# Kernel tuning notes

Measured on AMD Instinct MI355X. Metric: run time of the kernel, lower is better.

The kernel has to match this reference:

```python
import jax, jax.numpy as jnp
import numpy as np

ATT = 6  # att_size per axis
HEADS = 8

def leaky(x, s):
    return jnp.where(x >= 0, x, s * x)

def conv1x1(x, w, b):
    # x: [B,C,D,H,W], w: [O,C]
    return jnp.einsum('bcdhw,oc->bodhw', x, w) + b[None, :, None, None, None]

def conv3x3x3(x, w, b):
    y = jax.lax.conv_general_dilated(x, w, (1, 1, 1), [(1, 1)] * 3,
                                     dimension_numbers=('NCDHW', 'OIDHW', 'NCDHW'))
    return y + b[None, :, None, None, None]

def group_norm(x, g, b, groups=6, eps=1e-5):
    B, C = x.shape[:2]
    xr = x.reshape(B, groups, -1)
    m = xr.mean(-1, keepdims=True)
    v = xr.var(-1, keepdims=True)
    xr = (xr - m) * jax.lax.rsqrt(v + eps)
    return xr.reshape(x.shape) * g[None, :, None, None, None] + b[None, :, None, None, None]

def instance_norm(x, eps=1e-5):
    m = x.mean((2, 3, 4), keepdims=True)
    v = x.var((2, 3, 4), keepdims=True)
    return (x - m) * jax.lax.rsqrt(v + eps)

def pool_sum(x, out=ATT):
    # adaptive max + avg pool; spatial dims divisible by out -> exact block reduce
    B, C, D, H, W = x.shape
    f = D // out
    xr = x.reshape(B, C, out, f, out, f, out, f)
    return xr.max((3, 5, 7)) + xr.mean((3, 5, 7))

def interp_axis(x, axis, out_size):
    # 1D linear interp with align_corners=True
    in_size = x.shape[axis]
    pos = jnp.arange(out_size) * ((in_size - 1) / (out_size - 1))
    i0 = jnp.floor(pos).astype(jnp.int32)
    i1 = jnp.minimum(i0 + 1, in_size - 1)
    w = (pos - i0).astype(x.dtype)
    shp = [1] * x.ndim
    shp[axis] = out_size
    w = w.reshape(shp)
    return jnp.take(x, i0, axis=axis) * (1 - w) + jnp.take(x, i1, axis=axis) * w

def upsample_trilinear(x, size):
    for ax, s in zip((2, 3, 4), size):
        x = interp_axis(x, ax, s)
    return x

def lin_attn(q, k, v, wq, bq, wk, bk, wv, bv, wo, bo):
    # efficient (linear) cross-attention: softmax over feature dim for Q, token dim for K
    B, N, C = q.shape
    dh = C // HEADS
    qh = (jnp.einsum('bnc,oc->bno', q, wq) + bq).reshape(B, N, HEADS, dh)
    kh = (jnp.einsum('bnc,oc->bno', k, wk) + bk).reshape(B, N, HEADS, dh)
    vh = (jnp.einsum('bnc,oc->bno', v, wv) + bv).reshape(B, N, HEADS, dh)
    qs = jax.nn.softmax(qh, axis=-1)
    ks = jax.nn.softmax(kh, axis=1)
    ctx = jnp.einsum('bnhd,bnhe->bhde', ks, vh)      # [B,H,dh,dh]
    out = jnp.einsum('bnhd,bhde->bnhe', qs, ctx).reshape(B, N, C)
    out = jnp.einsum('bnc,oc->bno', out, wo) + bo
    return out.transpose(0, 2, 1)  # [B,C,N]

def deconv2(x, w, b):
    # ConvTranspose3d kernel=stride=2; w: [Cin,Cout,2,2,2]
    B, C, D, H, W = x.shape
    O = w.shape[1]
    y = jnp.einsum('bcdhw,coijk->bodihjwk', x, w).reshape(B, O, 2 * D, 2 * H, 2 * W)
    return y + b[None, :, None, None, None]

def setup_inputs():
    key = jax.random.key(0)
    ks = iter(jax.random.split(key, 48))
    nrm = lambda *s: jax.random.normal(next(ks), s, jnp.float32)
    w = lambda *s: nrm(*s) * 0.05
    d = {
        'x': nrm(4, 64, 24, 24, 24),
        'x_e': nrm(4, 32, 48, 48, 48),
        'up_w': w(64, 32, 2, 2, 2), 'up_b': w(32),
        'wf': w(48, 64), 'bf': w(48),
        'w1': w(48, 32), 'b1': w(48), 'w2': w(48, 32), 'b2': w(48),
        'w3': w(48, 48), 'b3': w(48), 'w4': w(48, 48), 'b4': w(48),
        'gn_g': jnp.ones(48, jnp.float32), 'gn_b': jnp.zeros(48, jnp.float32),
        'a1_wq': w(48, 48), 'a1_bq': w(48), 'a1_wk': w(48, 48), 'a1_bk': w(48),
        'a1_wv': w(48, 48), 'a1_bv': w(48), 'a1_wo': w(48, 48), 'a1_bo': w(48),
        'a2_wq': w(48, 48), 'a2_bq': w(48), 'a2_wk': w(48, 48), 'a2_bk': w(48),
        'a2_wv': w(48, 48), 'a2_bv': w(48), 'a2_wo': w(48, 48), 'a2_bo': w(48),
        'wfin': w(64, 96), 'bfin': w(64),
        'c0_w': w(32, 64, 3, 3, 3), 'c0_b': w(32),
        'c1_w': w(32, 32, 3, 3, 3), 'c1_b': w(32),
    }
    return d

def reference(x, x_e, up_w, up_b, wf, bf, w1, b1, w2, b2, w3, b3, w4, b4, gn_g, gn_b,
              a1_wq, a1_bq, a1_wk, a1_bk, a1_wv, a1_bv, a1_wo, a1_bo,
              a2_wq, a2_bq, a2_wk, a2_bk, a2_wv, a2_bv, a2_wo, a2_bo,
              wfin, bfin, c0_w, c0_b, c1_w, c1_b):
    x0 = deconv2(x, up_w, up_b)                                   # [B,32,48,48,48]
    fusion = conv1x1(jnp.concatenate([x_e, x0], 1), wf, bf)       # [B,48,...]
    B, C = fusion.shape[:2]
    i1 = leaky(group_norm(conv1x1(x0, w1, b1), gn_g, gn_b), 0.1)
    i1 = leaky(group_norm(conv1x1(i1, w3, b3), gn_g, gn_b), 0.1)
    i2 = leaky(group_norm(conv1x1(x_e, w2, b2), gn_g, gn_b), 0.1)
    i2 = leaky(group_norm(conv1x1(i2, w4, b4), gn_g, gn_b), 0.1)
    p1 = pool_sum(i1)
    p2 = pool_sum(i2)
    pkv = pool_sum(fusion)
    q1 = p1.reshape(B, C, -1).transpose(0, 2, 1)
    q2 = p2.reshape(B, C, -1).transpose(0, 2, 1)
    kv = pkv.reshape(B, C, -1).transpose(0, 2, 1)
    a1 = lin_attn(q1, kv, kv, a1_wq, a1_bq, a1_wk, a1_bk, a1_wv, a1_bv, a1_wo, a1_bo).reshape(B, C, ATT, ATT, ATT)
    a2 = lin_attn(q2, kv, kv, a2_wq, a2_bq, a2_wk, a2_bk, a2_wv, a2_bv, a2_wo, a2_bo).reshape(B, C, ATT, ATT, ATT)
    size = i1.shape[2:]
    o1 = jax.nn.sigmoid(upsample_trilinear(a1, size)) * i1
    o2 = jax.nn.sigmoid(upsample_trilinear(a2, size)) * i2
    out = conv1x1(jnp.concatenate([o1, o2], 1), wfin, bfin)       # [B,64,...]
    h = leaky(instance_norm(conv3x3x3(out, c0_w, c0_b)), 0.01)
    h = leaky(instance_norm(conv3x3x3(h, c1_w, c1_b)), 0.01)
    return h
```

## Files before the change

### kernel.cpp

```cpp
#include <hip/hip_runtime.h>
#include <hip/hip_bf16.h>

typedef __hip_bfloat16 bf16;
typedef __attribute__((ext_vector_type(8))) short short8x;
typedef __attribute__((ext_vector_type(4))) float f32x4;
typedef __attribute__((ext_vector_type(4))) unsigned int uint4x;

#define NV 110592
#define NVLL 110592ull
#define NSH 64
#define STSTRIDE 704

__device__ inline float ldmix(const void* p, size_t i, int f){
  return f ? ((const float*)p)[i] : __bfloat162float(((const bf16*)p)[i]);
}
__device__ inline float lo2f(unsigned int u){ union{unsigned int i; float f;} t; t.i = u<<16; return t.f; }
__device__ inline float hi2f(unsigned int u){ union{unsigned int i; float f;} t; t.i = u & 0xffff0000u; return t.f; }
__device__ inline unsigned short bfb(float f){ bf16 h=__float2bfloat16(f); unsigned short u; __builtin_memcpy(&u,&h,2); return u; }
__device__ inline unsigned int pk2(float a, float b){ return (unsigned int)bfb(a) | ((unsigned int)bfb(b)<<16); }

static const size_t BOFF_O1 = 2621440;
static const size_t BOFF_O2 = 45088768;
static const size_t BOFF_SP = 87556096;
static const size_t SLOT48  = 10616832;
#define SM_P1   0
#define SM_P2   41472
#define SM_PKV  82944
#define SM_A1   124416
#define SM_A2   165888
#define SM_ST   207360
#define SM_W    252416

#define W_UPW   0
#define W_UPB   16384
#define W_WF    16416
#define W_BF    19488
#define W_W1    19536
#define W_B1    21072
#define W_W2    21120
#define W_B2    22656
#define W_W3    22704
#define W_B3    25008
#define W_W4    25056
#define W_B4    27360
#define W_GNG   27408
#define W_GNB   27456
#define W_ATT   27504
#define W_WFIN  46320
#define W_BFIN  52464
#define W_C0W   52528
#define W_C0B   107824
#define W_C1W   107856
#define W_C1B   135504
#define W_TOTAL 135536
#define W_W1P   135536
#define W_B1F   160112
#define W_WFP   160160
#define W_BFF   184736
#define W_WP    184784
#define W_TB    267728
#define W_WB1   268592
#define W_WB2   310064
#define W_WB3   323888
#define W_WB4   324656
#define W_WB5   326192
#define W_WBI   327728
#define SM_FL   604720

__global__ __launch_bounds__(256) void k_detect(const void* xe, float* __restrict__ flag){
  const bf16* p = (const bf16*)xe;
  int tid = threadIdx.x;
  float mx = 0.f;
  for(int i=tid;i<8192;i+=256){
    float v = fabsf(__bfloat162float(p[i]));
    if(!(v==v)) v = 1e30f;
    mx = fmaxf(mx, v);
  }
  #pragma unroll
  for(int s=32;s>=1;s>>=1) mx = fmaxf(mx, __shfl_xor(mx,s));
  __shared__ float red[4];
  if((tid&63)==0) red[tid>>6] = mx;
  __syncthreads();
  if(tid==0){
    float m = fmaxf(fmaxf(red[0],red[1]), fmaxf(red[2],red[3]));
    flag[0] = (m > 1e3f) ? 1.f : 0.f;
  }
}

__global__ __launch_bounds__(256) void k_zero(float* __restrict__ st){
  int i = blockIdx.x*256 + threadIdx.x;
  if(i < NSH*STSTRIDE) st[i] = 0.f;
}

struct PtrTab { const void* p[36]; };
__device__ const int g_seg[36] = {16384,32,3072,48,1536,48,1536,48,2304,48,2304,48,48,48,
  2304,48,2304,48,2304,48,2304,48,2304,48,2304,48,2304,48,2304,48,6144,64,55296,32,27648,32};

__global__ __launch_bounds__(256) void k_prep(PtrTab t, float* __restrict__ W, const float* __restrict__ flag){
  const int f = (int)flag[0];
  int i = blockIdx.x*256 + threadIdx.x;
  if(i >= W_TOTAL) return;
  int rem = i;
  for(int s=0;s<36;s++){
    int sz = g_seg[s];
    if(rem < sz){ W[i] = ldmix(t.p[s], rem, f); return; }
    rem -= sz;
  }
}

__global__ __launch_bounds__(256) void k_fold(float* __restrict__ W){
  int i = blockIdx.x*256 + threadIdx.x;
  const float* upw = W + W_UPW;
  const float* upb = W + W_UPB;
  if(i < 49152){
    int which = i / 24576;
    int r = i % 24576;
    int par = r / 3072; int o = (r/64)%48; int c = r%64;
    float acc = 0.f;
    for(int m=0;m<32;m++){
      float wm = which ? W[W_WF + o*64 + 32 + m] : W[W_W1 + o*32 + m];
      acc += wm * upw[c*256 + m*8 + par];
    }
    W[(which ? W_WFP : W_W1P) + par*3072 + o*64 + c] = acc;
  } else if(i < 49248){
    int j = i - 49152;
    int which = j / 48; int o = j % 48;
    float acc = which ? W[W_BF + o] : W[W_B1 + o];
    for(int m=0;m<32;m++){
      float wm = which ? W[W_WF + o*64 + 32 + m] : W[W_W1 + o*32 + m];
      acc += wm * upb[m];
    }
    W[(which ? W_BFF : W_B1F) + o] = acc;
  }
}

__global__ __launch_bounds__(256) void k_fold2(float* __restrict__ W){
  int i = blockIdx.x*256 + threadIdx.x;
  if(i < 82944){
    int tap = i%27; int k = (i/27)%96; int oc = i/(27*96);
    float acc = 0.f;
    for(int m=0;m<64;m++) acc += W[W_C0W + oc*1728 + m*27 + tap] * W[W_WFIN + m*96 + k];
    W[W_WP + i] = acc;
  } else if(i < 83808){
    int j = i - 82944;
    int tap = j/32, oc = j%32;
    float acc = 0.f;
    for(int m=0;m<64;m++) acc += W[W_C0W + oc*1728 + m*27 + tap] * W[W_BFIN + m];
    W[W_TB + tap*32 + oc] = acc;
  }
}

__global__ __launch_bounds__(256) void k_packb1(float* __restrict__ W){
  int i = blockIdx.x*256 + threadIdx.x;
  if(i >= 82944) return;
  int j = i&7; int lane = (i>>3)&63; int frag = i>>9;
  int nt = frag&1; int tkt = frag>>1; int kt = tkt%3; int tap = tkt/3;
  int oc = nt*16 + (lane&15);
  int k  = kt*32 + ((lane>>4)<<3) + j;
  ((bf16*)(W + W_WB1))[i] = __float2bfloat16(W[W_WP + oc*2592 + k*27 + tap]);
}
__global__ __launch_bounds__(256) void k_packb2(float* __restrict__ W){
  int i = blockIdx.x*256 + threadIdx.x;
  if(i >= 27648) return;
  int j = i&7; int lane = (i>>3)&63; int frag = i>>9;
  int nt = frag&1; int tap = frag>>1;
  int oc = nt*16 + (lane&15);
  int ic = ((lane>>4)<<3) + j;
  ((bf16*)(W + W_WB2))[i] = __float2bfloat16(W[W_C1W + oc*864 + ic*27 + tap]);
}

__global__ __launch_bounds__(256) void k_packc(float* __restrict__ W, int srcoff, int cin, int ktc, int dstoff){
  int i = blockIdx.x*256 + threadIdx.x;
  if(i >= ktc*1536) return;
  int j=i&7, lane=(i>>3)&63, frag=i>>9;
  int nt = frag%3, kt = frag/3;
  int oc = nt*16 + (lane&15);
  int k  = kt*32 + ((lane>>4)<<3) + j;
  float v = (k < cin) ? W[srcoff + oc*cin + k] : 0.f;
  ((bf16*)(W + dstoff))[i] = __float2bfloat16(v);
}
__global__ __launch_bounds__(256) void k_packi1(float* __restrict__ W){
  int i = blockIdx.x*256 + threadIdx.x;
  if(i >= 24576) return;
  int j=i&7, lane=(i>>3)&63, frag=i>>9;
  int par = frag/6, rem = frag%6;
  int kt = rem/3, nt = rem%3;
  int oc = nt*16 + (lane&15);
  int k  = kt*32 + ((lane>>4)<<3) + j;
  ((bf16*)(W + W_WBI))[i] = __float2bfloat16(W[W_W1P + par*3072 + oc*64 + k]);
}

__global__ __launch_bounds__(256) void k_i1mm(const void* __restrict__ x, const float* __restrict__ W,
    bf16* __restrict__ out, float* __restrict__ stato, const float* __restrict__ flag)
{
  const int f = (int)flag[0];
  const int tid = threadIdx.x, wid = tid>>6, lane = tid&63;
  const int w = blockIdx.x*4 + wid;
  const int b = w/864, t = w%864;
  const int vc0 = t*16;
  const int m = lane&15, quad = lane>>4;
  const short8x* wbI = (const short8x*)(W + W_WBI);

  short8x ah[2], al[2];
  #pragma unroll
  for(int kt=0;kt<2;kt++){
    short hh[8], ll[8];
    #pragma unroll
    for(int j=0;j<8;j++){
      int k = kt*32 + quad*8 + j;
      float v = ldmix(x, ((size_t)(b*64 + k))*13824 + vc0 + m, f);
      bf16 h = __float2bfloat16(v);
      float hf = __bfloat162float(h);
      bf16 l = __float2bfloat16(v - hf);
      __builtin_memcpy(&hh[j], &h, 2); __builtin_memcpy(&ll[j], &l, 2);
    }
    __builtin_memcpy(&ah[kt], hh, 16); __builtin_memcpy(&al[kt], ll, 16);
  }

  f32x4 acc[8][3];
  #pragma unroll
  for(int p=0;p<8;p++)
    #pragma unroll
    for(int nt=0;nt<3;nt++) acc[p][nt] = (f32x4){0.f,0.f,0.f,0.f};

  #pragma unroll
  for(int par=0;par<8;par++){
    #pragma unroll
    for(int kt=0;kt<2;kt++){
      #pragma unroll
      for(int nt=0;nt<3;nt++){
        short8x bfr = wbI[(size_t)((par*2+kt)*3+nt)*64 + lane];
        acc[par][nt] = __builtin_amdgcn_mfma_f32_16x16x32_bf16(ah[kt], bfr, acc[par][nt], 0,0,0);
        acc[par][nt] = __builtin_amdgcn_mfma_f32_16x16x32_bf16(al[kt], bfr, acc[par][nt], 0,0,0);
      }
    }
  }

  __shared__ bf16 lds[4][128][48];
  __shared__ float sred[4][12];
  const float* bp = W + W_B1F;
  float sl[3] = {0,0,0}, ssl[3] = {0,0,0};
  #pragma unroll
  for(int nt=0;nt<3;nt++){
    int oc = nt*16 + m;
    float bias = bp[oc];
    #pragma unroll
    for(int par=0;par<8;par++){
      #pragma unroll
      for(int r=0;r<4;r++){
        float v = acc[par][nt][r] + bias;
        int vid = (quad*4+r)*8 + par;
        lds[wid][vid][oc] = __float2bfloat16(v);
        sl[nt] += v; ssl[nt] += v*v;
      }
    }
  }
  #pragma unroll
  for(int nt=0;nt<3;nt++){
    float a = sl[nt], s2 = ssl[nt];
    a += __shfl_xor(a,16); s2 += __shfl_xor(s2,16);
    a += __shfl_xor(a,32); s2 += __shfl_xor(s2,32);
    a += __shfl_xor(a,1);  s2 += __shfl_xor(s2,1);
    a += __shfl_xor(a,2);  s2 += __shfl_xor(s2,2);
    a += __shfl_xor(a,4);  s2 += __shfl_xor(s2,4);
    if(quad==0 && (m&7)==0){
      int g = nt*2 + (m>>3);
      sred[wid][g] = a; sred[wid][6+g] = s2;
    }
  }
  #pragma unroll
  for(int i=0;i<2;i++){
    int vid = lane*2 + i;
    int mm = vid>>3, par = vid&7;
    int vcm = vc0 + mm;
    int xh = vcm%24, yh = (vcm/24)%24, zh = vcm/576;
    int pz = par>>2, py = (par>>1)&1, px = par&1;
    size_t vout = (size_t)(2*zh+pz)*2304 + (2*yh+py)*48 + (2*xh+px);
    uint4x* dst = (uint4x*)(out + ((size_t)b*NVLL + vout)*48);
    const uint4x* srcl = (const uint4x*)&lds[wid][vid][0];
    #pragma unroll
    for(int q=0;q<6;q++) dst[q] = srcl[q];
  }
  __syncthreads();
  if(tid < 12){
    int bb = (blockIdx.x*4)/864;
    float v = sred[0][tid]+sred[1][tid]+sred[2][tid]+sred[3][tid];
    int g = tid%6, kind = tid/6;
    atomicAdd(&stato[(blockIdx.x&(NSH-1))*STSTRIDE + (kind?24:0) + bb*6+g], v);
  }
}

template<int CIN, bool MIX>
__global__ __launch_bounds__(256) void k_c1mm(const void* in, const bf16* __restrict__ wbf,
    const float* __restrict__ bias, bf16* out, float* __restrict__ stato, int set_out,
    const float* __restrict__ flag)
{
  constexpr int KT = (CIN+31)/32;
  const int f = MIX ? (int)flag[0] : 0;
  const int tid = threadIdx.x, wid = tid>>6, lane = tid&63;
  const int w = blockIdx.x*4 + wid;
  const size_t v0g = (size_t)w*16;
  const int b = (int)(v0g/NVLL);
  const size_t v0l = v0g - (size_t)b*NVLL;
  const int m = lane&15, quad = lane>>4;
  const short8x* wb8 = (const short8x*)wbf;
  const short8x zf = {0,0,0,0,0,0,0,0};

  short8x afh[KT], afl[MIX?KT:1];
  #pragma unroll
  for(int kt=0;kt<KT;kt++){
    if constexpr(MIX){
      short hh[8], ll[8];
      #pragma unroll
      for(int j=0;j<8;j++){
        int ch = kt*32 + quad*8 + j;
        float v = ldmix(in, ((size_t)(b*CIN+ch))*NVLL + v0l + m, f);
        bf16 h = __float2bfloat16(v);
        float hf = __bfloat162float(h);
        bf16 l = __float2bfloat16(v - hf);
        __builtin_memcpy(&hh[j], &h, 2); __builtin_memcpy(&ll[j], &l, 2);
      }
      __builtin_memcpy(&afh[kt], hh, 16); __builtin_memcpy(&afl[kt], ll, 16);
    } else {
      int k0 = kt*32 + quad*8;
      short8x a = (k0 < CIN) ? *(const short8x*)((const bf16*)in + (v0g + m)*48 + k0) : zf;
      afh[kt] = a;
    }
  }

  f32x4 acc[3];
  #pragma unroll
  for(int nt=0;nt<3;nt++) acc[nt] = (f32x4){0.f,0.f,0.f,0.f};
  #pragma unroll
  for(int kt=0;kt<KT;kt++){
    #pragma unroll
    for(int nt=0;nt<3;nt++){
      short8x bfr = wb8[(size_t)(kt*3+nt)*64 + lane];
      acc[nt] = __builtin_amdgcn_mfma_f32_16x16x32_bf16(afh[kt], bfr, acc[nt], 0,0,0);
      if constexpr(MIX)
        acc[nt] = __builtin_amdgcn_mfma_f32_16x16x32_bf16(afl[kt], bfr, acc[nt], 0,0,0);
    }
  }

  __shared__ bf16 lds[4][16][48];
  __shared__ float sred[4][12];
  float sl[3] = {0,0,0}, ssl[3] = {0,0,0};
  #pragma unroll
  for(int nt=0;nt<3;nt++){
    int oc = nt*16 + m;
    float bv = bias[oc];
    #pragma unroll
    for(int r=0;r<4;r++){
      float v = acc[nt][r] + bv;
      lds[wid][quad*4+r][oc] = __float2bfloat16(v);
      sl[nt] += v; ssl[nt] += v*v;
    }
  }
  #pragma unroll
  for(int nt=0;nt<3;nt++){
    float a = sl[nt], s2 = ssl[nt];
    a += __shfl_xor(a,16); s2 += __shfl_xor(s2,16);
    a += __shfl_xor(a,32); s2 += __shfl_xor(s2,32);
    a += __shfl_xor(a,1);  s2 += __shfl_xor(s2,1);
    a += __shfl_xor(a,2);  s2 += __shfl_xor(s2,2);
    a += __shfl_xor(a,4);  s2 += __shfl_xor(s2,4);
    if(quad==0 && (m&7)==0){
      int g = nt*2 + (m>>3);
      sred[wid][g] = a; sred[wid][6+g] = s2;
    }
  }
  if(lane < 16){
    uint4x* dst = (uint4x*)(out + (v0g + lane)*48);
    const uint4x* srcl = (const uint4x*)&lds[wid][lane][0];
    #pragma unroll
    for(int q=0;q<6;q++) dst[q] = srcl[q];
  }
  __syncthreads();
  if(tid < 12){
    int bb = (int)(((size_t)(blockIdx.x*4)*16)/NVLL);
    float v = sred[0][tid]+sred[1][tid]+sred[2][tid]+sred[3][tid];
    int g = tid%6, kind = tid/6;
    atomicAdd(&stato[(blockIdx.x&(NSH-1))*STSTRIDE + set_out*48 + (kind?24:0) + bb*6+g], v);
  }
}

__global__ __launch_bounds__(256) void k_gn_apply(bf16* buf, const float* __restrict__ stats, int set,
    const float* __restrict__ gamma, const float* __restrict__ beta)
{
  const int v = blockIdx.x*256 + threadIdx.x;
  const int b = blockIdx.y;
  __shared__ float sm[12];
  if(threadIdx.x < 12){
    int kind = threadIdx.x/6, g = threadIdx.x%6;
    int off = set*48 + (kind?24:0) + b*6+g;
    float s = 0.f;
    for(int sh=0; sh<NSH; sh++) s += stats[sh*STSTRIDE + off];
    sm[threadIdx.x] = s;
  }
  __syncthreads();
  const float invN = 1.0f/(8.0f*(float)NV);
  float m[6], rs[6];
  #pragma unroll
  for(int g=0;g<6;g++){
    float mm = sm[g]*invN;
    float var = sm[6+g]*invN - mm*mm;
    m[g] = mm; rs[g] = rsqrtf(var + 1e-5f);
  }
  uint4x* p4 = (uint4x*)(buf + ((size_t)b*NVLL + v)*48);
  uint4x w6[6];
  #pragma unroll
  for(int q=0;q<6;q++) w6[q] = p4[q];
  unsigned int* wu = (unsigned int*)w6;
  #pragma unroll
  for(int c2=0;c2<24;c2++){
    int c0 = 2*c2;
    float x0 = lo2f(wu[c2]), x1 = hi2f(wu[c2]);
    int g0 = c0>>3, g1 = (c0+1)>>3;
    x0 = (x0 - m[g0])*rs[g0]*gamma[c0] + beta[c0];
    x1 = (x1 - m[g1])*rs[g1]*gamma[c0+1] + beta[c0+1];
    x0 = x0 < 0.f ? 0.1f*x0 : x0;
    x1 = x1 < 0.f ? 0.1f*x1 : x1;
    wu[c2] = pk2(x0, x1);
  }
  #pragma unroll
  for(int q=0;q<6;q++) p4[q] = w6[q];
}

__global__ __launch_bounds__(512) void k_pool2(const bf16* __restrict__ s0, const bf16* __restrict__ s1,
    float* __restrict__ d0, float* __restrict__ d1)
{
  const int which = blockIdx.y;
  const bf16* src = which ? s1 : s0;
  float*      dst = which ? d1 : d0;
  const int cell = blockIdx.x % 216, b = blockIdx.x/216;
  const int tid = threadIdx.x;
  const int cz=cell/36, cy=(cell/6)%6, cx=cell%6;
  const int dz=tid>>6, dy=(tid>>3)&7, dx=tid&7;
  const size_t vox = (size_t)(cz*8+dz)*2304 + (cy*8+dy)*48 + (cx*8+dx);
  const uint4x* p4 = (const uint4x*)(src + ((size_t)b*NVLL + vox)*48);
  uint4x w6[6];
  #pragma unroll
  for(int q=0;q<6;q++) w6[q] = p4[q];
  const unsigned int* wu = (const unsigned int*)w6;
  float val[48];
  #pragma unroll
  for(int c2=0;c2<24;c2++){ val[2*c2] = lo2f(wu[c2]); val[2*c2+1] = hi2f(wu[c2]); }
  __shared__ float rmax[8][48], rsum[8][48];
  const int wid=tid>>6, lane=tid&63;
  #pragma unroll
  for(int o=0;o<48;o++){
    float mx=val[o], sm=val[o];
    #pragma unroll
    for(int s=32;s>=1;s>>=1){ mx=fmaxf(mx,__shfl_xor(mx,s)); sm+=__shfl_xor(sm,s); }
    if(lane==0){ rmax[wid][o]=mx; rsum[wid][o]=sm; }
  }
  __syncthreads();
  if(tid<48){
    float mx=rmax[0][tid], sm=rsum[0][tid];
    #pragma unroll
    for(int w2=1;w2<8;w2++){ mx=fmaxf(mx,rmax[w2][tid]); sm+=rsum[w2][tid]; }
    dst[(size_t)(b*48+tid)*216 + cell] = mx + sm*(1.f/512.f);
  }
}

__global__ __launch_bounds__(512) void k_poolfuse(const void* __restrict__ xe, const void* __restrict__ x,
    const float* __restrict__ W, float* __restrict__ pkv, const float* __restrict__ flag)
{
  const int f = (int)flag[0];
  const int cell = blockIdx.x % 216;
  const int b = blockIdx.x / 216;
  const int tid = threadIdx.x;
  const int cz = cell/36, cy = (cell/6)%6, cx = cell%6;
  const int dz = tid>>6, dy = (tid>>3)&7, dx = tid&7;
  const int gz = cz*8+dz, gy = cy*8+dy, gx = cx*8+dx;
  const size_t voff = (size_t)gz*2304 + gy*48 + gx;
  const int par = ((gz&1)<<2) | ((gy&1)<<1) | (gx&1);
  const int vh = (gz>>1)*576 + (gy>>1)*24 + (gx>>1);
  float xev[32], xrv[64];
  #pragma unroll
  for(int c=0;c<32;c++) xev[c] = ldmix(xe, ((size_t)(b*32+c))*NVLL + voff, f);
  #pragma unroll
  for(int c=0;c<64;c++) xrv[c] = ldmix(x, (size_t)(b*64+c)*13824 + vh, f);
  const float* wf  = W + W_WF;
  const float* wfp = W + W_WFP + par*3072;
  const float* bff = W + W_BFF;
  __shared__ float rmax[8][48];
  __shared__ float rsum[8][48];
  const int wid = tid>>6, lane = tid&63;
  #pragma unroll
  for(int o=0;o<48;o++){
    float acc = bff[o];
    #pragma unroll
    for(int c=0;c<32;c++) acc += wf[o*64+c]*xev[c];
    #pragma unroll
    for(int c=0;c<64;c++) acc += wfp[o*64+c]*xrv[c];
    float mx = acc, sm = acc;
    #pragma unroll
    for(int s=32;s>=1;s>>=1){ mx = fmaxf(mx, __shfl_xor(mx,s)); sm += __shfl_xor(sm,s); }
    if(lane==0){ rmax[wid][o] = mx; rsum[wid][o] = sm; }
  }
  __syncthreads();
  if(tid < 48){
    float mx = rmax[0][tid], sm = rsum[0][tid];
    #pragma unroll
    for(int w2=1;w2<8;w2++){ mx = fmaxf(mx, rmax[w2][tid]); sm += rsum[w2][tid]; }
    pkv[((size_t)(b*48+tid))*216 + cell] = mx + sm*(1.f/512.f);
  }
}

__global__ __launch_bounds__(256) void k_attn(const float* __restrict__ p1, const float* __restrict__ p2,
    const float* __restrict__ pkv, const float* __restrict__ W, float* __restrict__ a1, float* __restrict__ a2)
{
  const int which = blockIdx.x, b = blockIdx.y;
  const float* wb = W + W_ATT + which*9408;
  const float* wq = wb;        const float* bq = wb+2304;
  const float* wk = wb+2352;   const float* bk = wb+4656;
  const float* wv = wb+4704;   const float* bv = wb+7008;
  const float* wo = wb+7056;   const float* bo = wb+9360;
  const float* q   = which ? p2 : p1;
  float*       aout= which ? a2 : a1;
  const float* kvb = pkv + (size_t)b*48*216;
  const float* qb  = q   + (size_t)b*48*216;
  __shared__ float kh[216*48];
  __shared__ float ctx[288];
  const int tid = threadIdx.x;

  if(tid < 216){
    float kvr[48];
    #pragma unroll
    for(int c=0;c<48;c++) kvr[c] = kvb[c*216 + tid];
    #pragma unroll
    for(int o=0;o<48;o++){
      float acc = bk[o];
      #pragma unroll
      for(int c=0;c<48;c++) acc += kvr[c]*wk[o*48+c];
      kh[tid*48+o] = acc;
    }
  }
  __syncthreads();
  if(tid < 48){
    float mx = -1e30f;
    for(int n=0;n<216;n++) mx = fmaxf(mx, kh[n*48+tid]);
    float s = 0.f;
    for(int n=0;n<216;n++){ float e = __expf(kh[n*48+tid]-mx); kh[n*48+tid] = e; s += e; }
    float inv = 1.f/s;
    for(int n=0;n<216;n++) kh[n*48+tid] *= inv;
  }
  __syncthreads();
  if(tid < 48){
    int h = tid/6, e = tid%6;
    float cacc[6] = {0,0,0,0,0,0};
    for(int n=0;n<216;n++){
      float vh = bv[h*6+e];
      #pragma unroll
      for(int c=0;c<48;c++) vh += kvb[c*216+n]*wv[(h*6+e)*48+c];
      #pragma unroll
      for(int d=0;d<6;d++) cacc[d] += kh[n*48 + h*6+d]*vh;
    }
    #pragma unroll
    for(int d=0;d<6;d++) ctx[(h*6+d)*6+e] = cacc[d];
  }
  __syncthreads();
  if(tid < 216){
    int n = tid;
    float qr[48];
    #pragma unroll
    for(int c=0;c<48;c++) qr[c] = qb[c*216 + n];
    float qh[48];
    #pragma unroll
    for(int o=0;o<48;o++){
      float acc = bq[o];
      #pragma unroll
      for(int c=0;c<48;c++) acc += qr[c]*wq[o*48+c];
      qh[o] = acc;
    }
    #pragma unroll
    for(int h=0;h<8;h++){
      float mx = qh[h*6];
      #pragma unroll
      for(int d=1;d<6;d++) mx = fmaxf(mx, qh[h*6+d]);
      float s = 0.f;
      #pragma unroll
      for(int d=0;d<6;d++){ float e = __expf(qh[h*6+d]-mx); qh[h*6+d] = e; s += e; }
      float inv = 1.f/s;
      #pragma unroll
      for(int d=0;d<6;d++) qh[h*6+d] *= inv;
    }
    float ov[48];
    #pragma unroll
    for(int h=0;h<8;h++){
      #pragma unroll
      for(int e=0;e<6;e++){
        float acc = 0.f;
        #pragma unroll
        for(int d=0;d<6;d++) acc += qh[h*6+d]*ctx[(h*6+d)*6+e];
        ov[h*6+e] = acc;
      }
    }
    #pragma unroll
    for(int o=0;o<48;o++){
      float acc = bo[o];
      #pragma unroll
      for(int c=0;c<48;c++) acc += ov[c]*wo[o*48+c];
      aout[((size_t)(b*48+o))*216 + n] = acc;
    }
  }
}

__device__ inline void interp1(int u, int& i0, int& i1, float& t){
  float pos = u * (5.0f/47.0f);
  float f = floorf(pos);
  i0 = (int)f; if(i0 > 5) i0 = 5;
  i1 = i0+1 > 5 ? 5 : i0+1;
  t = pos - f; if(t < 0.f) t = 0.f; if(t > 1.f) t = 1.f;
}

__global__ __launch_bounds__(256) void k_gate(bf16* i1b, bf16* i2b,
    const float* __restrict__ a1, const float* __restrict__ a2)
{
  const int v = blockIdx.x*256 + threadIdx.x;
  const int b = blockIdx.y;
  const int x = v % 48, y = (v/48) % 48, z = v/2304;
  int xi0,xi1,yi0,yi1,zi0,zi1; float xt,yt,zt;
  interp1(x,xi0,xi1,xt); interp1(y,yi0,yi1,yt); interp1(z,zi0,zi1,zt);
  int off[8]; float cw[8];
  off[0]=zi0*36+yi0*6+xi0; cw[0]=(1-zt)*(1-yt)*(1-xt);
  off[1]=zi0*36+yi0*6+xi1; cw[1]=(1-zt)*(1-yt)*xt;
  off[2]=zi0*36+yi1*6+xi0; cw[2]=(1-zt)*yt*(1-xt);
  off[3]=zi0*36+yi1*6+xi1; cw[3]=(1-zt)*yt*xt;
  off[4]=zi1*36+yi0*6+xi0; cw[4]=zt*(1-yt)*(1-xt);
  off[5]=zi1*36+yi0*6+xi1; cw[5]=zt*(1-yt)*xt;
  off[6]=zi1*36+yi1*6+xi0; cw[6]=zt*yt*(1-xt);
  off[7]=zi1*36+yi1*6+xi1; cw[7]=zt*yt*xt;
  const float* A1b = a1 + (size_t)b*48*216;
  const float* A2b = a2 + (size_t)b*48*216;

  uint4x* p14 = (uint4x*)(i1b + ((size_t)b*NVLL + v)*48);
  uint4x* p24 = (uint4x*)(i2b + ((size_t)b*NVLL + v)*48);
  uint4x w6[6];
  #pragma unroll
  for(int q=0;q<6;q++) w6[q] = p14[q];
  unsigned int* wu = (unsigned int*)w6;
  #pragma unroll
  for(int c2=0;c2<24;c2++){
    int c0 = 2*c2;
    float s0 = 0.f, s1 = 0.f;
    #pragma unroll
    for(int k=0;k<8;k++){ s0 += cw[k]*A1b[c0*216+off[k]]; s1 += cw[k]*A1b[(c0+1)*216+off[k]]; }
    s0 = 1.f/(1.f + __expf(-s0));
    s1 = 1.f/(1.f + __expf(-s1));
    wu[c2] = pk2(s0*lo2f(wu[c2]), s1*hi2f(wu[c2]));
  }
  #pragma unroll
  for(int q=0;q<6;q++) p14[q] = w6[q];

  #pragma unroll
  for(int q=0;q<6;q++) w6[q] = p24[q];
  #pragma unroll
  for(int c2=0;c2<24;c2++){
    int c0 = 2*c2;
    float s0 = 0.f, s1 = 0.f;
    #pragma unroll
    for(int k=0;k<8;k++){ s0 += cw[k]*A2b[c0*216+off[k]]; s1 += cw[k]*A2b[(c0+1)*216+off[k]]; }
    s0 = 1.f/(1.f + __expf(-s0));
    s1 = 1.f/(1.f + __expf(-s1));
    wu[c2] = pk2(s0*lo2f(wu[c2]), s1*hi2f(wu[c2]));
  }
  #pragma unroll
  for(int q=0;q<6;q++) p24[q] = w6[q];
}

template<int KT, bool TWO, bool USETB>
__global__ __launch_bounds__(256) void k_conv3m(
    const bf16* __restrict__ in0, const bf16* __restrict__ in1,
    const bf16* __restrict__ wb, const float* __restrict__ tb, const float* __restrict__ cb,
    bf16* __restrict__ outp, float* __restrict__ stato, int sOut, int bidx, int onhwc)
{
  const int tid = threadIdx.x;
  const int wid = tid>>6, lane = tid&63;
  const int run = blockIdx.x*4 + wid;
  const int x0 = (run%3)*16, y = (run/3)%48, z = run/144;
  const int m = lane&15, quad = lane>>4;
  const int CB = TWO ? 48 : 32;
  const int k0 = quad*8;
  const short8x* wb8 = (const short8x*)wb;
  const short8x zf = {0,0,0,0,0,0,0,0};

  f32x4 acc0 = {0.f,0.f,0.f,0.f};
  f32x4 acc1 = {0.f,0.f,0.f,0.f};

  for(int dz=0; dz<3; dz++){
    int zz = z + dz - 1;
    if(zz < 0 || zz >= 48) continue;
    for(int dy=0; dy<3; dy++){
      int yy = y + dy - 1;
      if(yy < 0 || yy >= 48) continue;
      #pragma unroll
      for(int dx=0; dx<3; dx++){
        int xx = x0 + m + dx - 1;
        bool ok = (xx >= 0 && xx < 48);
        int xc = xx < 0 ? 0 : (xx > 47 ? 47 : xx);
        int vox = zz*2304 + yy*48 + xc;
        int tap = dz*9 + dy*3 + dx;
        #pragma unroll
        for(int kt=0; kt<KT; kt++){
          int kk = kt*32 + k0;
          const bf16* src; int ch;
          if(TWO){ if(kk < 48){ src = in0; ch = kk; } else { src = in1; ch = kk-48; } }
          else    { src = in0; ch = kk; }
          short8x af = *(const short8x*)(src + (size_t)vox*CB + ch);
          if(!ok) af = zf;
          short8x b0 = wb8[ (size_t)((tap*KT + kt)*2 + 0)*64 + lane ];
          short8x b1 = wb8[ (size_t)((tap*KT + kt)*2 + 1)*64 + lane ];
          acc0 = __builtin_amdgcn_mfma_f32_16x16x32_bf16(af, b0, acc0, 0,0,0);
          acc1 = __builtin_amdgcn_mfma_f32_16x16x32_bf16(af, b1, acc1, 0,0,0);
        }
      }
    }
  }

  const int oc0 = m, oc1 = 16 + m;
  float s0=0.f, ss0=0.f, s1=0.f, ss1=0.f;
  #pragma unroll
  for(int r=0;r<4;r++){
    int mv = quad*4 + r;
    int xr = x0 + mv;
    float b0v = cb[oc0], b1v = cb[oc1];
    if constexpr(USETB){
      #pragma unroll
      for(int t=0;t<27;t++){
        int tdz = t/9, tdy = (t/3)%3, tdx = t%3;
        int zz = z+tdz-1, yy = y+tdy-1, xx = xr+tdx-1;
        if(zz>=0 && zz<48 && yy>=0 && yy<48 && xx>=0 && xx<48){
          b0v += tb[t*32+oc0]; b1v += tb[t*32+oc1];
        }
      }
    }
    float v0 = acc0[r] + b0v;
    float v1 = acc1[r] + b1v;
    size_t vox = (size_t)z*2304 + y*48 + xr;
    if(onhwc){
      outp[vox*32 + oc0] = __float2bfloat16(v0);
      outp[vox*32 + oc1] = __float2bfloat16(v1);
    } else {
      outp[(size_t)oc0*NVLL + vox] = __float2bfloat16(v0);
      outp[(size_t)oc1*NVLL + vox] = __float2bfloat16(v1);
    }
    s0 += v0; ss0 += v0*v0; s1 += v1; ss1 += v1*v1;
  }
  s0 += __shfl_xor(s0,16); ss0 += __shfl_xor(ss0,16); s1 += __shfl_xor(s1,16); ss1 += __shfl_xor(ss1,16);
  s0 += __shfl_xor(s0,32); ss0 += __shfl_xor(ss0,32); s1 += __shfl_xor(s1,32); ss1 += __shfl_xor(ss1,32);
  __shared__ float csum[4][32], css[4][32];
  if(quad==0){
    csum[wid][oc0]=s0; css[wid][oc0]=ss0;
    csum[wid][oc1]=s1; css[wid][oc1]=ss1;
  }
  __syncthreads();
  if(tid < 64){
    int oc = tid&31, kind = tid>>5;
    float v = kind ? (css[0][oc]+css[1][oc]+css[2][oc]+css[3][oc])
                   : (csum[0][oc]+csum[1][oc]+csum[2][oc]+csum[3][oc]);
    atomicAdd(&stato[(blockIdx.x&(NSH-1))*STSTRIDE + sOut + (kind?128:0) + bidx*32 + oc], v);
  }
}

struct P4 { bf16* p[4]; };
__global__ __launch_bounds__(256) void k_inleak(P4 h1, const float* __restrict__ stats){
  int gid = blockIdx.x*256 + threadIdx.x;
  int b = gid/NV; int v = gid - b*NV;
  __shared__ float sm2[64];
  if(threadIdx.x < 64){
    int oc = threadIdx.x&31, kind = threadIdx.x>>5;
    int off = 192 + (kind?128:0) + b*32 + oc;
    float s = 0.f;
    for(int sh=0; sh<NSH; sh++) s += stats[sh*STSTRIDE + off];
    sm2[threadIdx.x] = s;
  }
  __syncthreads();
  const float invN = 1.f/(float)NV;
  uint4x* p4 = (uint4x*)(h1.p[b] + (size_t)v*32);
  uint4x w4[4];
  #pragma unroll
  for(int q=0;q<4;q++) w4[q] = p4[q];
  unsigned int* wu = (unsigned int*)w4;
  #pragma unroll
  for(int c2=0;c2<16;c2++){
    int c0 = 2*c2;
    float m0 = sm2[c0]*invN,   m1 = sm2[c0+1]*invN;
    float r0 = rsqrtf(sm2[32+c0]*invN - m0*m0 + 1e-5f);
    float r1 = rsqrtf(sm2[32+c0+1]*invN - m1*m1 + 1e-5f);
    float x0 = (lo2f(wu[c2]) - m0)*r0;
    float x1 = (hi2f(wu[c2]) - m1)*r1;
    x0 = x0 < 0.f ? 0.01f*x0 : x0;
    x1 = x1 < 0.f ? 0.01f*x1 : x1;
    wu[c2] = pk2(x0, x1);
  }
  #pragma unroll
  for(int q=0;q<4;q++) p4[q] = w4[q];
}

__global__ __launch_bounds__(256) void k_in_final(P4 h2, const float* __restrict__ stats,
    void* out, const float* __restrict__ flag)
{
  const int f = (int)flag[0];
  int gid = blockIdx.x*256 + threadIdx.x;
  size_t i8 = (size_t)gid*8;
  int b = (int)(i8/(NV*32)); int j = (int)(i8 - (size_t)b*(NV*32));
  int c = j/NV;
  size_t i80 = (size_t)(blockIdx.x*256)*8;
  int b0 = (int)(i80/(NV*32)); int j0 = (int)(i80 - (size_t)b0*(NV*32));
  int c0 = j0/NV;
  __shared__ float sm2[4];
  if(threadIdx.x < 4){
    int dc = threadIdx.x>>1, kind = threadIdx.x&1;
    int cc = c0+dc > 31 ? 31 : c0+dc;
    int off = 448 + (kind?128:0) + b0*32 + cc;
    float s = 0.f;
    for(int sh=0; sh<NSH; sh++) s += stats[sh*STSTRIDE + off];
    sm2[threadIdx.x] = s;
  }
  __syncthreads();
  const float invN = 1.f/(float)NV;
  int dc = c - c0;
  float m = sm2[dc*2]*invN;
  float var = sm2[dc*2+1]*invN - m*m;
  float rs = rsqrtf(var + 1e-5f);
  uint4x w = *(uint4x*)(h2.p[b] + j);
  const unsigned int* wu = (const unsigned int*)&w;
  float vv[8];
  #pragma unroll
  for(int k2=0;k2<4;k2++){ vv[2*k2] = lo2f(wu[k2]); vv[2*k2+1] = hi2f(wu[k2]); }
  #pragma unroll
  for(int k=0;k<8;k++){
    float xv = (vv[k]-m)*rs;
    vv[k] = xv < 0.f ? 0.01f*xv : xv;
  }
  if(f){
    float* op = (float*)out + i8;
    uint4x o0, o1;
    __builtin_memcpy(&o0, &vv[0], 16);
    __builtin_memcpy(&o1, &vv[4], 16);
    ((uint4x*)op)[0] = o0; ((uint4x*)op)[1] = o1;
  } else {
    unsigned int pk[4];
    #pragma unroll
    for(int k2=0;k2<4;k2++) pk[k2] = pk2(vv[2*k2], vv[2*k2+1]);
    *(uint4x*)((bf16*)out + i8) = *(uint4x*)pk;
  }
}

extern "C" void kernel_launch(void* const* d_in, const int* in_sizes, int n_in,
                              void* d_out, int out_size, void* d_ws, size_t ws_size,
                              hipStream_t stream)
{
  (void)in_sizes; (void)n_in; (void)out_size; (void)ws_size;
  char* base = (char*)d_ws;
  const void* x  = d_in[0];
  const void* xe = d_in[1];

  float* SM  = (float*)base;
  float* P1  = SM + SM_P1;
  float* P2  = SM + SM_P2;
  float* PKV = SM + SM_PKV;
  float* A1  = SM + SM_A1;
  float* A2  = SM + SM_A2;
  float* ST  = SM + SM_ST;
  float* W   = SM + SM_W;
  float* FL  = SM + SM_FL;
  bf16*  O1  = (bf16*)(base + BOFF_O1);
  bf16*  O2  = (bf16*)(base + BOFF_O2);

  P4 H1, H2;
  H1.p[0] = (bf16*)(base + BOFF_SP);
  H1.p[1] = (bf16*)(base + BOFF_O1);
  H1.p[2] = (bf16*)(base + BOFF_O1 + SLOT48);
  H1.p[3] = (bf16*)(base + BOFF_O1 + 2*SLOT48);
  for(int b=0;b<4;b++) H2.p[b] = (bf16*)(base + BOFF_O2 + (size_t)b*SLOT48);

  k_detect<<<1, 256, 0, stream>>>(xe, FL);
  k_zero<<<(NSH*STSTRIDE+255)/256, 256, 0, stream>>>(ST);

  PtrTab pt;
  for(int i=0;i<36;i++) pt.p[i] = d_in[i+2];
  k_prep<<<(W_TOTAL+255)/256, 256, 0, stream>>>(pt, W, FL);
  k_fold <<<193, 256, 0, stream>>>(W);
  k_fold2<<<328, 256, 0, stream>>>(W);
  k_packb1<<<324, 256, 0, stream>>>(W);
  k_packb2<<<108, 256, 0, stream>>>(W);
  k_packc<<<6,  256, 0, stream>>>(W, W_W2, 32, 1, W_WB3);
  k_packc<<<12, 256, 0, stream>>>(W, W_W3, 48, 2, W_WB4);
  k_packc<<<12, 256, 0, stream>>>(W, W_W4, 48, 2, W_WB5);
  k_packi1<<<96, 256, 0, stream>>>(W);

  const float* gam = W + W_GNG;
  const float* bet = W + W_GNB;

  k_i1mm<<<864, 256, 0, stream>>>(x, W, O1, ST, FL);
  k_gn_apply<<<dim3(432,4), 256, 0, stream>>>(O1, ST, 0, gam, bet);
  k_c1mm<48,false><<<6912, 256, 0, stream>>>(O1, (const bf16*)(W+W_WB4), W+W_B3, O1, ST, 1, FL);
  k_gn_apply<<<dim3(432,4), 256, 0, stream>>>(O1, ST, 1, gam, bet);

  k_c1mm<32,true ><<<6912, 256, 0, stream>>>(xe, (const bf16*)(W+W_WB3), W+W_B2, O2, ST, 2, FL);
  k_gn_apply<<<dim3(432,4), 256, 0, stream>>>(O2, ST, 2, gam, bet);
  k_c1mm<48,false><<<6912, 256, 0, stream>>>(O2, (const bf16*)(W+W_WB5), W+W_B4, O2, ST, 3, FL);
  k_gn_apply<<<dim3(432,4), 256, 0, stream>>>(O2, ST, 3, gam, bet);

  k_pool2<<<dim3(864,2), 512, 0, stream>>>(O1, O2, P1, P2);
  k_poolfuse<<<864, 512, 0, stream>>>(xe, x, W, PKV, FL);
  k_attn<<<dim3(2,4), 256, 0, stream>>>(P1, P2, PKV, W, A1, A2);

  k_gate<<<dim3(432,4), 256, 0, stream>>>(O1, O2, A1, A2);

  for(int b=0;b<4;b++){
    const bf16* o1b = O1 + (size_t)b*48*NVLL;
    const bf16* o2b = O2 + (size_t)b*48*NVLL;
    k_conv3m<3,true,true><<<1728, 256, 0, stream>>>(o1b, o2b, (const bf16*)(W+W_WB1), W+W_TB, W+W_C0B,
                                                    H1.p[b], ST, 192, b, 1);
  }
  k_inleak<<<1728, 256, 0, stream>>>(H1, ST);

  for(int b=0;b<4;b++){
    k_conv3m<1,false,false><<<1728, 256, 0, stream>>>(H1.p[b], nullptr, (const bf16*)(W+W_WB2), nullptr, W+W_C1B,
                                                      H2.p[b], ST, 448, b, 0);
  }
  k_in_final<<<6912, 256, 0, stream>>>(H2, ST, d_out, FL);
}
```

Before: 1.817 ms.

## Fuse group-norm apply into following 1x1 conv and regroup poolfuse threads by parity

Drops two standalone group-norm apply passes over the 48-channel bf16 activations. The following 1x1 MFMA conv instead sums the per-shard stats, then normalizes and applies leaky-ReLU to its input fragments as it loads them, saving a full read and write of two large tensors. Separately, the pool-fuse kernel maps each wavefront to one parity class, so the parity-specific weight pointer is uniform per wave and the upsampled low-res reads are shared. Risks include extra per-block stat reduction work (64 shards), per-element gamma/beta loads in the conv, and in-place O1/O2 updates where blocks read and write the same rows.

```diff
diff --git a/kernel.cpp b/kernel.cpp
--- a/kernel.cpp
+++ b/kernel.cpp
@@ -290,9 +290,11 @@
   }
 }
 
-template<int CIN, bool MIX>
+template<int CIN, bool MIX, bool GNIN>
 __global__ __launch_bounds__(256) void k_c1mm(const void* in, const bf16* __restrict__ wbf,
     const float* __restrict__ bias, bf16* out, float* __restrict__ stato, int set_out,
+    const float* __restrict__ stats_in, int set_in,
+    const float* __restrict__ gamma, const float* __restrict__ beta,
     const float* __restrict__ flag)
 {
   constexpr int KT = (CIN+31)/32;
@@ -306,6 +308,29 @@
   const short8x* wb8 = (const short8x*)wbf;
   const short8x zf = {0,0,0,0,0,0,0,0};
 
+  __shared__ float gsm[12];
+  if constexpr(GNIN){
+    if(tid < 12){
+      int bb = (int)(((size_t)blockIdx.x*64)/NVLL);
+      int kind = tid/6, g = tid%6;
+      int off = set_in*48 + (kind?24:0) + bb*6+g;
+      float s = 0.f;
+      for(int sh=0; sh<NSH; sh++) s += stats_in[sh*STSTRIDE + off];
+      gsm[tid] = s;
+    }
+    __syncthreads();
+  }
+  float gm[GNIN?6:1], gr[GNIN?6:1];
+  if constexpr(GNIN){
+    const float invN = 1.0f/(8.0f*(float)NV);
+    #pragma unroll
+    for(int g=0;g<6;g++){
+      float mm = gsm[g]*invN;
+      float var = gsm[6+g]*invN - mm*mm;
+      gm[g] = mm; gr[g] = rsqrtf(var + 1e-5f);
+    }
+  }
+
   short8x afh[KT], afl[MIX?KT:1];
   #pragma unroll
   for(int kt=0;kt<KT;kt++){
@@ -323,8 +348,25 @@
       __builtin_memcpy(&afh[kt], hh, 16); __builtin_memcpy(&afl[kt], ll, 16);
     } else {
       int k0 = kt*32 + quad*8;
-      short8x a = (k0 < CIN) ? *(const short8x*)((const bf16*)in + (v0g + m)*48 + k0) : zf;
-      afh[kt] = a;
+      if(k0 < CIN){
+        short8x a = *(const short8x*)((const bf16*)in + (v0g + m)*48 + k0);
+        if constexpr(GNIN){
+          short hh[8];
+          #pragma unroll
+          for(int j=0;j<8;j++){
+            int ch = k0 + j;
+            short raw = a[j];
+            unsigned int u = ((unsigned int)(unsigned short)raw) << 16;
+            float xv; __builtin_memcpy(&xv, &u, 4);
+            int g = ch>>3;
+            xv = (xv - gm[g])*gr[g]*gamma[ch] + beta[ch];
+            xv = xv < 0.f ? 0.1f*xv : xv;
+            hh[j] = (short)bfb(xv);
+          }
+          __builtin_memcpy(&a, hh, 16);
+        }
+        afh[kt] = a;
+      } else afh[kt] = zf;
     }
   }
 
@@ -470,23 +512,23 @@
   const int cell = blockIdx.x % 216;
   const int b = blockIdx.x / 216;
   const int tid = threadIdx.x;
+  const int wid = tid>>6, lane = tid&63;
+  const int pz = wid>>2, py = (wid>>1)&1, px = wid&1;
   const int cz = cell/36, cy = (cell/6)%6, cx = cell%6;
-  const int dz = tid>>6, dy = (tid>>3)&7, dx = tid&7;
-  const int gz = cz*8+dz, gy = cy*8+dy, gx = cx*8+dx;
-  const size_t voff = (size_t)gz*2304 + gy*48 + gx;
-  const int par = ((gz&1)<<2) | ((gy&1)<<1) | (gx&1);
-  const int vh = (gz>>1)*576 + (gy>>1)*24 + (gx>>1);
+  const int czi = lane>>4, cyi = (lane>>2)&3, cxi = lane&3;
+  const int zc = cz*4+czi, yc = cy*4+cyi, xc = cx*4+cxi;
+  const int vh = zc*576 + yc*24 + xc;
+  const size_t voff = (size_t)(2*zc+pz)*2304 + (2*yc+py)*48 + (2*xc+px);
   float xev[32], xrv[64];
   #pragma unroll
   for(int c=0;c<32;c++) xev[c] = ldmix(xe, ((size_t)(b*32+c))*NVLL + voff, f);
   #pragma unroll
   for(int c=0;c<64;c++) xrv[c] = ldmix(x, (size_t)(b*64+c)*13824 + vh, f);
   const float* wf  = W + W_WF;
-  const float* wfp = W + W_WFP + par*3072;
+  const float* wfp = W + W_WFP + wid*3072;
   const float* bff = W + W_BFF;
   __shared__ float rmax[8][48];
   __shared__ float rsum[8][48];
-  const int wid = tid>>6, lane = tid&63;
   #pragma unroll
   for(int o=0;o<48;o++){
     float acc = bff[o];
@@ -896,13 +938,11 @@
   const float* bet = W + W_GNB;
 
   k_i1mm<<<864, 256, 0, stream>>>(x, W, O1, ST, FL);
-  k_gn_apply<<<dim3(432,4), 256, 0, stream>>>(O1, ST, 0, gam, bet);
-  k_c1mm<48,false><<<6912, 256, 0, stream>>>(O1, (const bf16*)(W+W_WB4), W+W_B3, O1, ST, 1, FL);
+  k_c1mm<48,false,true ><<<6912, 256, 0, stream>>>(O1, (const bf16*)(W+W_WB4), W+W_B3, O1, ST, 1, ST, 0, gam, bet, FL);
   k_gn_apply<<<dim3(432,4), 256, 0, stream>>>(O1, ST, 1, gam, bet);
 
-  k_c1mm<32,true ><<<6912, 256, 0, stream>>>(xe, (const bf16*)(W+W_WB3), W+W_B2, O2, ST, 2, FL);
-  k_gn_apply<<<dim3(432,4), 256, 0, stream>>>(O2, ST, 2, gam, bet);
-  k_c1mm<48,false><<<6912, 256, 0, stream>>>(O2, (const bf16*)(W+W_WB5), W+W_B4, O2, ST, 3, FL);
+  k_c1mm<32,true ,false><<<6912, 256, 0, stream>>>(xe, (const bf16*)(W+W_WB3), W+W_B2, O2, ST, 2, ST, 0, gam, bet, FL);
+  k_c1mm<48,false,true ><<<6912, 256, 0, stream>>>(O2, (const bf16*)(W+W_WB5), W+W_B4, O2, ST, 3, ST, 2, gam, bet, FL);
   k_gn_apply<<<dim3(432,4), 256, 0, stream>>>(O2, ST, 3, gam, bet);
 
   k_pool2<<<dim3(864,2), 512, 0, stream>>>(O1, O2, P1, P2);
```

New measurement: 1.692 ms. -6.9%, faster.
